# Kernel tuning notes

Hardware: AMD Instinct MI355X
Metric: run time of the kernel (lower is better)

The kernel has to match this reference:

```python
import jax, jax.numpy as jnp
import numpy as np
from jax import lax

EPS = 0.1        # entropic regularization
MAX_ITER = 100   # Sinkhorn iteration budget
THRESH = 0.1     # early-stop threshold on err = mean_b sum_i |u - u_prev|
B, N, D = 16, 1024, 64


def setup_inputs() -> dict:
    key = jax.random.key(0)
    k1, k2 = jax.random.split(key)
    x = jax.random.normal(k1, (B, N, D), dtype=jnp.float32)
    y = jax.random.normal(k2, (B, N, D), dtype=jnp.float32)
    return {"x": x, "y": y}


def _lse(A):
    # Faithful to the original (unstabilized) lse: log(sum(exp(A)) + 1e-6)
    return jnp.log(jnp.exp(A).sum(-1) + 1e-6)


def _M(C, u, v):
    # (-C_ij + u_i + v_j) / eps
    return (-C + u[..., :, None] + v[..., None, :]) / EPS


def _cost_matrix(x, y):
    # (avoids materializing the [B, N, N, D] difference tensor; same math for p=2)
    x2 = (x * x).sum(-1)                         # [B, N]
    y2 = (y * y).sum(-1)                         # [B, N]
    xy = jnp.einsum('bid,bjd->bij', x, y)        # [B, N, N]
    return x2[..., :, None] + y2[..., None, :] - 2.0 * xy


def reference(x, y):
    x = jax.nn.softmax(x, axis=-1)
    y = jax.nn.softmax(y, axis=-1)
    C = _cost_matrix(x, y)                       # [B, N, N]
    n = x.shape[-2]
    log_mu = jnp.log(1.0 / n + 1e-8)             # mu = nu = uniform 1/n (scalar broadcast)
    u0 = jnp.zeros((x.shape[0], n), dtype=C.dtype)
    v0 = jnp.zeros_like(u0)

    def cond(carry):
        _, _, i, err = carry
        return jnp.logical_and(i < MAX_ITER, err >= THRESH)

    def body(carry):
        u, v, i, _ = carry
        u1 = u
        u = EPS * (log_mu - _lse(_M(C, u, v))) + u
        v = EPS * (log_mu - _lse(jnp.swapaxes(_M(C, u, v), -2, -1))) + v
        err = jnp.abs(u - u1).sum(-1).mean()
        return (u, v, i + 1, err)

    u, v, _, _ = lax.while_loop(
        cond, body, (u0, v0, jnp.int32(0), jnp.float32(jnp.inf)))

    pi = jnp.exp(_M(C, u, v))                    # transport plan [B, N, N]
    cost = (pi * C).sum((-2, -1))                # [B]
    return cost.mean()                           # reduction='mean'
```

## Files before the change

kernel.cpp:

```cpp
#include <hip/hip_runtime.h>
#include <hip/hip_bf16.h>
#include <math.h>

#define BATCH 16
#define NPTS 1024
#define DIM 64
#define EPSF 0.1f
#define INV_EPS 10.0f
#define MAX_ITER 100
#define THRESHF 0.1f
#define LSTRIDE 72

typedef _Float16 h8 __attribute__((ext_vector_type(8)));
typedef short short8v __attribute__((ext_vector_type(8)));
typedef float float4v __attribute__((ext_vector_type(4)));

#define ATOMIC_ST(p, v) \
  __hip_atomic_store((p), (v), __ATOMIC_RELAXED, __HIP_MEMORY_SCOPE_AGENT)
#define ATOMIC_LD(p) \
  __hip_atomic_load((p), __ATOMIC_RELAXED, __HIP_MEMORY_SCOPE_AGENT)

__device__ inline float waveSum(float x) {
#pragma unroll
  for (int off = 32; off; off >>= 1) x += __shfl_xor(x, off, 64);
  return x;
}
__device__ inline float waveMax(float x) {
#pragma unroll
  for (int off = 32; off; off >>= 1) x = fmaxf(x, __shfl_xor(x, off, 64));
  return x;
}

__global__ __launch_bounds__(512, 2) void sinkhorn_fused(
    const float* __restrict__ x, const float* __restrict__ y,
    __hip_bfloat16* __restrict__ syh,
    float* __restrict__ y2,
    float* __restrict__ colsum,
    float* __restrict__ deltaPub,
    float* __restrict__ errB,
    int* __restrict__ flags,
    float* __restrict__ costPart,
    float* __restrict__ out) {
  __shared__ __attribute__((aligned(16))) short xs[64 * LSTRIDE];
  __shared__ __attribute__((aligned(16))) short ys[2][64 * LSTRIDE];
  __shared__ __attribute__((aligned(16))) short os[2][64 * LSTRIDE];
  __shared__ __attribute__((aligned(16))) float wLDS[NPTS];
  __shared__ __attribute__((aligned(16))) float vLDS[NPTS];
  __shared__ __attribute__((aligned(16))) float colpart[8][NPTS];
  __shared__ float x2L[64];
  __shared__ float derr[8];
  __shared__ float errbL[BATCH];
  const int t = threadIdx.x;
  const int blk = blockIdx.x;
  const int wave = t >> 6, lane = t & 63;
  const int batch = (blk & 7) + 8 * (blk >> 7);
  const int kslot = (blk >> 3) & 15;
  const float log_mu = logf(1.0f / 1024.0f + 1e-8f);

#pragma unroll
  for (int rr = 0; rr < 8; rr++) {
    int rl = wave * 8 + rr;
    int gr = batch * NPTS + kslot * 64 + rl;
    float xv = x[(size_t)gr * DIM + lane];
    float mx = waveMax(xv);
    float ex = expf(xv - mx);
    float sx = waveSum(ex);
    float px = ex / sx;
    __hip_bfloat16 hbx = (__hip_bfloat16)px;
    xs[rl * LSTRIDE + lane] = *(const short*)&hbx;
    float sqx = waveSum(px * px);
    if (lane == 0) x2L[rl] = sqx;
    float yv = y[(size_t)gr * DIM + lane];
    float my = waveMax(yv);
    float ey = expf(yv - my);
    float sy = waveSum(ey);
    float py = ey / sy;
    __hip_bfloat16 hby = (__hip_bfloat16)py;
    unsigned bits = *(const unsigned short*)&hby;
    unsigned nb = __shfl_down(bits, 1);
    if ((lane & 1) == 0)
      ATOMIC_ST((unsigned*)((unsigned short*)syh + (size_t)gr * DIM + lane),
                bits | (nb << 16));
    float sqy = waveSum(py * py);
    if (lane == 0) ATOMIC_ST(&y2[gr], sqy);
  }
  if (t < 192) {
    int buf = t >> 6, j = kslot * 64 + (t & 63);
    ATOMIC_ST(&colsum[((size_t)buf * BATCH + batch) * NPTS + j], 0.f);
  }
  __syncthreads();
  if (t == 0) ATOMIC_ST(&flags[batch * 16 + kslot], 1);
  if (t < 16) {
    while (ATOMIC_LD(&flags[batch * 16 + t]) < 1) {}
  }
  __syncthreads();

  const int m = lane & 15, q = lane >> 4;
  const int g = lane >> 3, sub = lane & 7;
  const int sw = wave & 3, ts = wave >> 2;
  short8v a0 = *(const short8v*)&xs[(sw * 16 + m) * LSTRIDE + q * 8];
  short8v a1 = *(const short8v*)&xs[(sw * 16 + m) * LSTRIDE + 32 + q * 8];
  float xa[4];
#pragma unroll
  for (int reg = 0; reg < 4; reg++) xa[reg] = x2L[sw * 16 + q * 4 + reg];
  float kaf[8][16];
#pragma unroll
  for (int k = 0; k < 8; k++) {
    {
      int idx = t;
#pragma unroll
      for (int rep = 0; rep < 2; rep++, idx += 512) {
        int r = idx >> 3, c = idx & 7;
        *(short8v*)&ys[r >> 6][(r & 63) * LSTRIDE + c * 8] = *(const short8v*)(
            (const short*)syh + ((size_t)batch * NPTS + 128 * k + r) * DIM + c * 8);
      }
    }
    __syncthreads();
    const int jt = 2 * k + ts;
    float4v accv[4];
#pragma unroll
    for (int tj = 0; tj < 4; tj++) {
      short8v b0 = *(const short8v*)&ys[ts][(tj * 16 + m) * LSTRIDE + q * 8];
      short8v b1 = *(const short8v*)&ys[ts][(tj * 16 + m) * LSTRIDE + 32 + q * 8];
      float4v c = {0.f, 0.f, 0.f, 0.f};
      c = __builtin_amdgcn_mfma_f32_16x16x32_bf16(a0, b0, c, 0, 0, 0);
      c = __builtin_amdgcn_mfma_f32_16x16x32_bf16(a1, b1, c, 0, 0, 0);
      accv[tj] = c;
    }
#pragma unroll
    for (int tj = 0; tj < 4; tj++) {
      float y2v = y2[(size_t)batch * NPTS + jt * 64 + tj * 16 + m];
#pragma unroll
      for (int reg = 0; reg < 4; reg++) {
        float C = xa[reg] + y2v - 2.0f * accv[tj][reg];
        _Float16 kv = (_Float16)expf(-INV_EPS * C);
        os[ts][(sw * 16 + q * 4 + reg) * LSTRIDE + tj * 16 + m] = *(const short*)&kv;
      }
    }
    __syncthreads();
    {
      int e0 = (2 * k) & 7, e1 = (2 * k + 1) & 7;
      if (g == e0 || g == e1) {
        const short* srcp = (g == e0) ? &os[0][0] : &os[1][0];
#pragma unroll
        for (int rr = 0; rr < 8; rr++) {
          h8 v = *(const h8*)&srcp[(wave * 8 + rr) * LSTRIDE + sub * 8];
#pragma unroll
          for (int n = 0; n < 8; n++) {
            if (k < 4) kaf[rr][n] = (float)v[n];
            else kaf[rr][8 + n] = (float)v[n];
          }
        }
      }
    }
    __syncthreads();
  }

  for (int j = t; j < NPTS; j += 512) { vLDS[j] = 0.f; wLDS[j] = 1.f; }
  __syncthreads();

  float u[8], uPrev[8], eu[8];
#pragma unroll
  for (int r = 0; r < 8; r++) { u[r] = 0.f; eu[r] = 1.f; }
  int it = 0;

  while (true) {
#pragma unroll
    for (int r = 0; r < 8; r++) uPrev[r] = u[r];
    const float4* w4 = (const float4*)wLDS;
    float wreg[16];
    *(float4*)&wreg[0]  = w4[2 * lane];
    *(float4*)&wreg[4]  = w4[2 * lane + 1];
    *(float4*)&wreg[8]  = w4[128 + 2 * lane];
    *(float4*)&wreg[12] = w4[128 + 2 * lane + 1];
    float colreg[16];
#pragma unroll
    for (int n = 0; n < 16; n++) colreg[n] = 0.f;
    float delta = 0.f;
#pragma unroll
    for (int rr = 0; rr < 8; rr++) {
      float dot = 0.f;
#pragma unroll
      for (int n = 0; n < 16; n++) dot = fmaf(kaf[rr][n], wreg[n], dot);
      dot = waveSum(dot);
      float uo = u[rr];
      float s = eu[rr] * dot;
      float un = EPSF * (log_mu - logf(s + 1e-6f)) + uo;
      delta += fabsf(un - uo);
      u[rr] = un;
      float ai = expf(INV_EPS * un);
      eu[rr] = ai;
#pragma unroll
      for (int n = 0; n < 16; n++) colreg[n] = fmaf(kaf[rr][n], ai, colreg[n]);
    }
    if (lane == 0) derr[wave] = delta;
    {
      float4* cp = (float4*)&colpart[wave][0];
      cp[2 * lane]       = make_float4(colreg[0], colreg[1], colreg[2], colreg[3]);
      cp[2 * lane + 1]   = make_float4(colreg[4], colreg[5], colreg[6], colreg[7]);
      cp[128 + 2 * lane] = make_float4(colreg[8], colreg[9], colreg[10], colreg[11]);
      cp[128 + 2 * lane + 1] = make_float4(colreg[12], colreg[13], colreg[14], colreg[15]);
    }
    __syncthreads();
    float* cs = colsum + ((size_t)(it % 3) * BATCH + batch) * NPTS;
#pragma unroll
    for (int rep = 0; rep < 2; rep++) {
      int j = t + rep * 512;
      float s = 0.f;
#pragma unroll
      for (int w = 0; w < 8; w++) s += colpart[w][j];
      unsafeAtomicAdd(&cs[j], s);
    }
    if (t == 0) {
      float e = 0.f;
#pragma unroll
      for (int w = 0; w < 8; w++) e += derr[w];
      ATOMIC_ST(&deltaPub[((it & 1) * BATCH + batch) * 16 + kslot], e);
    }
    __syncthreads();
    if (t == 0) ATOMIC_ST(&flags[batch * 16 + kslot], it + 2);
    float errPre = -1.0f;
    if (it >= 1 && t < BATCH)
      errPre = ATOMIC_LD(&errB[(it - 1) * BATCH + t]);
    if (t < 16) {
      while (ATOMIC_LD(&flags[batch * 16 + t]) < it + 2) {}
    }
    __syncthreads();
    float cs0 = ATOMIC_LD(&cs[t]);
    float cs1 = ATOMIC_LD(&cs[t + 512]);
    if (t < 64)
      ATOMIC_ST(&colsum[((size_t)((it + 2) % 3) * BATCH + batch) * NPTS +
                        kslot * 64 + t], 0.f);
    if (kslot == 0 && t == 0) {
      const float* dp = deltaPub + ((it & 1) * BATCH + batch) * 16;
      float e = 0.f;
#pragma unroll
      for (int k = 0; k < 16; k++) e += ATOMIC_LD((float*)&dp[k]);
      ATOMIC_ST(&errB[it * BATCH + batch], e);
    }
    if (it >= 1) {
      if (t < BATCH) {
        float v = errPre;
        while (v < 0.f) v = ATOMIC_LD(&errB[(it - 1) * BATCH + t]);
        errbL[t] = v;
      }
      __syncthreads();
      float errv = 0.f;
#pragma unroll
      for (int k = 0; k < BATCH; k++) errv += errbL[k];
      if (errv * (1.0f / (float)BATCH) < THRESHF) {
#pragma unroll
        for (int r = 0; r < 8; r++) u[r] = uPrev[r];
        break;
      }
    }
    {
      float ev0 = wLDS[t];
      float vo = vLDS[t];
      float s = ev0 * cs0;
      float vn = EPSF * (log_mu - logf(s + 1e-6f)) + vo;
      vLDS[t] = vn;
      wLDS[t] = expf(INV_EPS * vn);
      float ev1 = wLDS[t + 512];
      float vo1 = vLDS[t + 512];
      float s1 = ev1 * cs1;
      float vn1 = EPSF * (log_mu - logf(s1 + 1e-6f)) + vo1;
      vLDS[t + 512] = vn1;
      wLDS[t + 512] = expf(INV_EPS * vn1);
    }
    it++;
    if (it >= MAX_ITER) break;
    __syncthreads();
  }

  {
    __syncthreads();
    const float4* w4 = (const float4*)wLDS;
    float wreg[16];
    *(float4*)&wreg[0]  = w4[2 * lane];
    *(float4*)&wreg[4]  = w4[2 * lane + 1];
    *(float4*)&wreg[8]  = w4[128 + 2 * lane];
    *(float4*)&wreg[12] = w4[128 + 2 * lane + 1];
    float csum = 0.f;
#pragma unroll
    for (int rr = 0; rr < 8; rr++) {
      float ai = expf(INV_EPS * u[rr]);
#pragma unroll
      for (int n = 0; n < 16; n++) {
        float kf = kaf[rr][n];
        if (kf > 0.f)
          csum += ai * wreg[n] * kf * (-EPSF * logf(kf));
      }
    }
    csum = waveSum(csum);
    if (lane == 0) derr[wave] = csum;
    __syncthreads();
    if (t == 0) {
      float cst = 0.f;
#pragma unroll
      for (int w = 0; w < 8; w++) cst += derr[w];
      ATOMIC_ST(&costPart[blk], cst + 1.0f);
    }
    if (blk == 0) {
      if (t < 256) {
        float v;
        while ((v = ATOMIC_LD(&costPart[t])) < 0.5f) {}
        colpart[0][t] = v;
      }
      __syncthreads();
      if (wave == 0) {
        float s = colpart[0][lane] + colpart[0][lane + 64] +
                  colpart[0][lane + 128] + colpart[0][lane + 192];
        s = waveSum(s);
        if (lane == 0) out[0] = (s - 256.0f) * (1.0f / (float)BATCH);
      }
    }
  }
}

extern "C" void kernel_launch(void* const* d_in, const int* in_sizes, int n_in,
                              void* d_out, int out_size, void* d_ws,
                              size_t ws_size, hipStream_t stream) {
  (void)in_sizes; (void)n_in; (void)out_size; (void)ws_size;
  const float* x = (const float*)d_in[0];
  const float* y = (const float*)d_in[1];
  float* out = (float*)d_out;

  char* ws = (char*)d_ws;
  size_t off = 0;
  auto alloc = [&](size_t nbytes) -> void* {
    void* p = (void*)(ws + off);
    off = (off + nbytes + 255) & ~(size_t)255;
    return p;
  };
  __hip_bfloat16* syh = (__hip_bfloat16*)alloc((size_t)BATCH * NPTS * DIM * 2);
  float* y2 = (float*)alloc((size_t)BATCH * NPTS * 4);
  float* colsum = (float*)alloc((size_t)3 * BATCH * NPTS * 4);
  float* deltaPub = (float*)alloc((size_t)2 * BATCH * 16 * 4);
  float* errB = (float*)alloc((size_t)MAX_ITER * BATCH * 4);
  int* flags = (int*)alloc((size_t)BATCH * 16 * 4);
  float* costPart = (float*)alloc(256 * 4);

  void* args[] = {&x, &y, &syh, &y2, &colsum, &deltaPub,
                  &errB, &flags, &costPart, &out};
  hipLaunchCooperativeKernel((void*)sinkhorn_fused, dim3(256), dim3(512), args,
                             0, stream);
}
```

Measured before the change: 134.9 us.

## Pack per-block error into 64-bit flag word and iterate in exp domain

Each block's partial error is packed into the low half of a 64-bit flag store. This removes the separate deltaPub array and the extra barrier that came before the flag publish. The wait on the previous iteration's error is moved ahead of the barrier, and atomic-add column order is staggered by kslot to spread contention. The u/v updates are rewritten in the scaling (exp) domain using rcp instead of log/exp per element, and fast __expf/__logf intrinsics are used throughout. Risks are reduced numerical accuracy and subtle ordering changes in the cross-block protocol.

```diff
diff --git a/kernel.cpp b/kernel.cpp
--- a/kernel.cpp
+++ b/kernel.cpp
@@ -36,16 +36,14 @@
     __hip_bfloat16* __restrict__ syh,
     float* __restrict__ y2,
     float* __restrict__ colsum,
-    float* __restrict__ deltaPub,
+    long long* __restrict__ flags,
     float* __restrict__ errB,
-    int* __restrict__ flags,
     float* __restrict__ costPart,
     float* __restrict__ out) {
   __shared__ __attribute__((aligned(16))) short xs[64 * LSTRIDE];
   __shared__ __attribute__((aligned(16))) short ys[2][64 * LSTRIDE];
   __shared__ __attribute__((aligned(16))) short os[2][64 * LSTRIDE];
   __shared__ __attribute__((aligned(16))) float wLDS[NPTS];
-  __shared__ __attribute__((aligned(16))) float vLDS[NPTS];
   __shared__ __attribute__((aligned(16))) float colpart[8][NPTS];
   __shared__ float x2L[64];
   __shared__ float derr[8];
@@ -56,6 +54,7 @@
   const int batch = (blk & 7) + 8 * (blk >> 7);
   const int kslot = (blk >> 3) & 15;
   const float log_mu = logf(1.0f / 1024.0f + 1e-8f);
+  const float mu_c = 1.0f / 1024.0f + 1e-8f;
 
 #pragma unroll
   for (int rr = 0; rr < 8; rr++) {
@@ -63,7 +62,7 @@
     int gr = batch * NPTS + kslot * 64 + rl;
     float xv = x[(size_t)gr * DIM + lane];
     float mx = waveMax(xv);
-    float ex = expf(xv - mx);
+    float ex = __expf(xv - mx);
     float sx = waveSum(ex);
     float px = ex / sx;
     __hip_bfloat16 hbx = (__hip_bfloat16)px;
@@ -72,7 +71,7 @@
     if (lane == 0) x2L[rl] = sqx;
     float yv = y[(size_t)gr * DIM + lane];
     float my = waveMax(yv);
-    float ey = expf(yv - my);
+    float ey = __expf(yv - my);
     float sy = waveSum(ey);
     float py = ey / sy;
     __hip_bfloat16 hby = (__hip_bfloat16)py;
@@ -89,9 +88,9 @@
     ATOMIC_ST(&colsum[((size_t)buf * BATCH + batch) * NPTS + j], 0.f);
   }
   __syncthreads();
-  if (t == 0) ATOMIC_ST(&flags[batch * 16 + kslot], 1);
+  if (t == 0) ATOMIC_ST(&flags[batch * 16 + kslot], (long long)1 << 32);
   if (t < 16) {
-    while (ATOMIC_LD(&flags[batch * 16 + t]) < 1) {}
+    while ((int)(ATOMIC_LD(&flags[batch * 16 + t]) >> 32) < 1) {}
   }
   __syncthreads();
 
@@ -133,7 +132,7 @@
 #pragma unroll
       for (int reg = 0; reg < 4; reg++) {
         float C = xa[reg] + y2v - 2.0f * accv[tj][reg];
-        _Float16 kv = (_Float16)expf(-INV_EPS * C);
+        _Float16 kv = (_Float16)__expf(-INV_EPS * C);
         os[ts][(sw * 16 + q * 4 + reg) * LSTRIDE + tj * 16 + m] = *(const short*)&kv;
       }
     }
@@ -156,17 +155,17 @@
     __syncthreads();
   }
 
-  for (int j = t; j < NPTS; j += 512) { vLDS[j] = 0.f; wLDS[j] = 1.f; }
+  for (int j = t; j < NPTS; j += 512) wLDS[j] = 1.f;
   __syncthreads();
 
-  float u[8], uPrev[8], eu[8];
-#pragma unroll
-  for (int r = 0; r < 8; r++) { u[r] = 0.f; eu[r] = 1.f; }
+  float eu[8], euPrev[8];
+#pragma unroll
+  for (int r = 0; r < 8; r++) eu[r] = 1.f;
   int it = 0;
 
   while (true) {
 #pragma unroll
-    for (int r = 0; r < 8; r++) uPrev[r] = u[r];
+    for (int r = 0; r < 8; r++) euPrev[r] = eu[r];
     const float4* w4 = (const float4*)wLDS;
     float wreg[16];
     *(float4*)&wreg[0]  = w4[2 * lane];
@@ -183,12 +182,10 @@
 #pragma unroll
       for (int n = 0; n < 16; n++) dot = fmaf(kaf[rr][n], wreg[n], dot);
       dot = waveSum(dot);
-      float uo = u[rr];
-      float s = eu[rr] * dot;
-      float un = EPSF * (log_mu - logf(s + 1e-6f)) + uo;
-      delta += fabsf(un - uo);
-      u[rr] = un;
-      float ai = expf(INV_EPS * un);
+      float sp = eu[rr] * dot + 1e-6f;
+      float lg = __logf(sp);
+      delta += fabsf(EPSF * (log_mu - lg));
+      float ai = mu_c * eu[rr] * __builtin_amdgcn_rcpf(sp);
       eu[rr] = ai;
 #pragma unroll
       for (int n = 0; n < 16; n++) colreg[n] = fmaf(kaf[rr][n], ai, colreg[n]);
@@ -203,27 +200,44 @@
     }
     __syncthreads();
     float* cs = colsum + ((size_t)(it % 3) * BATCH + batch) * NPTS;
-#pragma unroll
-    for (int rep = 0; rep < 2; rep++) {
-      int j = t + rep * 512;
-      float s = 0.f;
-#pragma unroll
-      for (int w = 0; w < 8; w++) s += colpart[w][j];
-      unsafeAtomicAdd(&cs[j], s);
-    }
+    {
+      int j0 = (t + (kslot << 6)) & 1023;
+      int j1 = j0 ^ 512;
+      float s0 = 0.f, s1 = 0.f;
+#pragma unroll
+      for (int w = 0; w < 8; w++) { s0 += colpart[w][j0]; s1 += colpart[w][j1]; }
+      unsafeAtomicAdd(&cs[j0], s0);
+      unsafeAtomicAdd(&cs[j1], s1);
+    }
+    if (it >= 1 && t < BATCH) {
+      float v;
+      while ((v = ATOMIC_LD(&errB[(it - 1) * BATCH + t])) < 0.f) {}
+      errbL[t] = v;
+    }
+    float eblk = 0.f;
     if (t == 0) {
-      float e = 0.f;
-#pragma unroll
-      for (int w = 0; w < 8; w++) e += derr[w];
-      ATOMIC_ST(&deltaPub[((it & 1) * BATCH + batch) * 16 + kslot], e);
-    }
-    __syncthreads();
-    if (t == 0) ATOMIC_ST(&flags[batch * 16 + kslot], it + 2);
-    float errPre = -1.0f;
-    if (it >= 1 && t < BATCH)
-      errPre = ATOMIC_LD(&errB[(it - 1) * BATCH + t]);
+#pragma unroll
+      for (int w = 0; w < 8; w++) eblk += derr[w];
+    }
+    __syncthreads();
+    if (t == 0)
+      ATOMIC_ST(&flags[batch * 16 + kslot],
+                ((long long)(it + 2) << 32) | (long long)__float_as_uint(eblk));
+    if (it >= 1) {
+      float errv = 0.f;
+#pragma unroll
+      for (int k = 0; k < BATCH; k++) errv += errbL[k];
+      if (errv * (1.0f / (float)BATCH) < THRESHF) {
+#pragma unroll
+        for (int r = 0; r < 8; r++) eu[r] = euPrev[r];
+        break;
+      }
+    }
+    float dpoll = 0.f;
     if (t < 16) {
-      while (ATOMIC_LD(&flags[batch * 16 + t]) < it + 2) {}
+      long long fw;
+      while ((int)((fw = ATOMIC_LD(&flags[batch * 16 + t])) >> 32) < it + 2) {}
+      dpoll = __uint_as_float((unsigned)fw);
     }
     __syncthreads();
     float cs0 = ATOMIC_LD(&cs[t]);
@@ -231,42 +245,17 @@
     if (t < 64)
       ATOMIC_ST(&colsum[((size_t)((it + 2) % 3) * BATCH + batch) * NPTS +
                         kslot * 64 + t], 0.f);
-    if (kslot == 0 && t == 0) {
-      const float* dp = deltaPub + ((it & 1) * BATCH + batch) * 16;
-      float e = 0.f;
-#pragma unroll
-      for (int k = 0; k < 16; k++) e += ATOMIC_LD((float*)&dp[k]);
-      ATOMIC_ST(&errB[it * BATCH + batch], e);
-    }
-    if (it >= 1) {
-      if (t < BATCH) {
-        float v = errPre;
-        while (v < 0.f) v = ATOMIC_LD(&errB[(it - 1) * BATCH + t]);
-        errbL[t] = v;
-      }
-      __syncthreads();
-      float errv = 0.f;
-#pragma unroll
-      for (int k = 0; k < BATCH; k++) errv += errbL[k];
-      if (errv * (1.0f / (float)BATCH) < THRESHF) {
-#pragma unroll
-        for (int r = 0; r < 8; r++) u[r] = uPrev[r];
-        break;
-      }
-    }
-    {
-      float ev0 = wLDS[t];
-      float vo = vLDS[t];
-      float s = ev0 * cs0;
-      float vn = EPSF * (log_mu - logf(s + 1e-6f)) + vo;
-      vLDS[t] = vn;
-      wLDS[t] = expf(INV_EPS * vn);
-      float ev1 = wLDS[t + 512];
-      float vo1 = vLDS[t + 512];
-      float s1 = ev1 * cs1;
-      float vn1 = EPSF * (log_mu - logf(s1 + 1e-6f)) + vo1;
-      vLDS[t + 512] = vn1;
-      wLDS[t + 512] = expf(INV_EPS * vn1);
+    if (wave == 0) {
+      float e16 = (lane < 16) ? dpoll : 0.f;
+#pragma unroll
+      for (int off = 8; off; off >>= 1) e16 += __shfl_xor(e16, off, 16);
+      if (t == 0 && kslot == 0) ATOMIC_ST(&errB[it * BATCH + batch], e16);
+    }
+    {
+      float w0 = wLDS[t];
+      wLDS[t] = mu_c * w0 * __builtin_amdgcn_rcpf(w0 * cs0 + 1e-6f);
+      float w1 = wLDS[t + 512];
+      wLDS[t + 512] = mu_c * w1 * __builtin_amdgcn_rcpf(w1 * cs1 + 1e-6f);
     }
     it++;
     if (it >= MAX_ITER) break;
@@ -284,12 +273,12 @@
     float csum = 0.f;
 #pragma unroll
     for (int rr = 0; rr < 8; rr++) {
-      float ai = expf(INV_EPS * u[rr]);
+      float ai = eu[rr];
 #pragma unroll
       for (int n = 0; n < 16; n++) {
         float kf = kaf[rr][n];
         if (kf > 0.f)
-          csum += ai * wreg[n] * kf * (-EPSF * logf(kf));
+          csum += ai * wreg[n] * kf * (-EPSF * __logf(kf));
       }
     }
     csum = waveSum(csum);
@@ -336,13 +325,12 @@
   __hip_bfloat16* syh = (__hip_bfloat16*)alloc((size_t)BATCH * NPTS * DIM * 2);
   float* y2 = (float*)alloc((size_t)BATCH * NPTS * 4);
   float* colsum = (float*)alloc((size_t)3 * BATCH * NPTS * 4);
-  float* deltaPub = (float*)alloc((size_t)2 * BATCH * 16 * 4);
+  long long* flags = (long long*)alloc((size_t)BATCH * 16 * 8);
   float* errB = (float*)alloc((size_t)MAX_ITER * BATCH * 4);
-  int* flags = (int*)alloc((size_t)BATCH * 16 * 4);
   float* costPart = (float*)alloc(256 * 4);
 
-  void* args[] = {&x, &y, &syh, &y2, &colsum, &deltaPub,
-                  &errB, &flags, &costPart, &out};
+  void* args[] = {&x, &y, &syh, &y2, &colsum, &flags,
+                  &errB, &costPart, &out};
   hipLaunchCooperativeKernel((void*)sinkhorn_fused, dim3(256), dim3(512), args,
                              0, stream);
 }
```

Measured after the change: 131.6 us. 2.5% less time.
